# Kernel tuning notes

Hardware: AMD Instinct MI355X
Metric: run time of the kernel (lower is better)

## Reference

```python
import jax, jax.numpy as jnp
import numpy as np

N, E, D_IN, H, C, D_OUT = 50000, 800000, 16, 4, 64, 32


def setup_inputs() -> dict:
    key = jax.random.key(0)
    ks = jax.random.split(key, 24)
    w = lambda k, shape: (jax.random.normal(k, shape, jnp.float32) * 0.1)
    p = {}
    p["x"] = jax.random.normal(ks[0], (N, D_IN), jnp.float32)
    p["edge_index"] = jax.random.randint(ks[1], (2, E), 0, N, jnp.int32)
    p["W1"] = w(ks[2], (D_IN, H * C))
    p["a1_src"] = w(ks[3], (H, C))
    p["a1_dst"] = w(ks[4], (H, C))
    p["b1"] = jnp.zeros((H * C,), jnp.float32)
    p["W2"] = w(ks[5], (H * C, H * C))
    p["a2_src"] = w(ks[6], (H, C))
    p["a2_dst"] = w(ks[7], (H, C))
    p["b2"] = jnp.zeros((H * C,), jnp.float32)
    # GATConv 3: 256 -> 32, 1 head, concat=False (mean)
    p["W3"] = w(ks[8], (H * C, 1 * D_OUT))
    p["a3_src"] = w(ks[9], (1, D_OUT))
    p["a3_dst"] = w(ks[10], (1, D_OUT))
    p["b3"] = jnp.zeros((D_OUT,), jnp.float32)
    # LayerNorms over 256
    p["g1"] = jnp.ones((H * C,), jnp.float32)
    p["beta1"] = jnp.zeros((H * C,), jnp.float32)
    p["g2"] = jnp.ones((H * C,), jnp.float32)
    p["beta2"] = jnp.zeros((H * C,), jnp.float32)
    # risk head: Linear(32,32) -> ReLU -> Linear(32,6) -> Sigmoid
    p["Wr1"] = w(ks[11], (D_OUT, 32))
    p["br1"] = jnp.zeros((32,), jnp.float32)
    p["Wr2"] = w(ks[12], (32, 6))
    p["br2"] = jnp.zeros((6,), jnp.float32)
    return p


def layernorm(x, g, b, eps=1e-5):
    mu = jnp.mean(x, axis=-1, keepdims=True)
    var = jnp.mean(jnp.square(x - mu), axis=-1, keepdims=True)
    return (x - mu) * jax.lax.rsqrt(var + eps) * g + b


def gat_layer(x, src, dst, W, b, a_src, a_dst, n_nodes, concat):
    # PyG GATConv (eval mode): lin -> per-edge leaky_relu score -> segment softmax over dst -> scatter sum
    heads, ch = a_src.shape
    h = (x @ W).reshape(n_nodes, heads, ch)                 # [N,H,C]
    alpha_s = jnp.sum(h * a_src[None], axis=-1)             # [N,H]
    alpha_d = jnp.sum(h * a_dst[None], axis=-1)             # [N,H]
    e = jax.nn.leaky_relu(alpha_s[src] + alpha_d[dst], 0.2)  # [E,H]
    m = jax.ops.segment_max(e, dst, num_segments=n_nodes)   # stable softmax per dst
    ex = jnp.exp(e - m[dst])
    denom = jax.ops.segment_sum(ex, dst, num_segments=n_nodes)
    alpha = ex / (denom[dst] + 1e-16)                        # [E,H]
    out = jax.ops.segment_sum(alpha[:, :, None] * h[src], dst, num_segments=n_nodes)  # [N,H,C]
    out = out.reshape(n_nodes, heads * ch) if concat else out.mean(axis=1)
    return out + b


def reference(x, edge_index, W1, a1_src, a1_dst, b1, W2, a2_src, a2_dst, b2,
              W3, a3_src, a3_dst, b3, g1, beta1, g2, beta2, Wr1, br1, Wr2, br2):
    n = x.shape[0]
    loops = jnp.arange(n, dtype=edge_index.dtype)
    src = jnp.concatenate([edge_index[0], loops])  # GATConv adds self-loops by default
    dst = jnp.concatenate([edge_index[1], loops])
    h = gat_layer(x, src, dst, W1, b1, a1_src, a1_dst, n, True)
    h = jax.nn.elu(layernorm(h, g1, beta1))
    h = gat_layer(h, src, dst, W2, b2, a2_src, a2_dst, n, True)
    h = jax.nn.elu(layernorm(h, g2, beta2))
    h = gat_layer(h, src, dst, W3, b3, a3_src, a3_dst, n, False)
    risk = jax.nn.sigmoid(jax.nn.relu(h @ Wr1 + br1) @ Wr2 + br2)
    return (h, risk)
```

## Files before the change

### kernel.cpp

```cpp
#include <hip/hip_runtime.h>
#include <hip/hip_bf16.h>
#include <cmath>

constexpr int Nn  = 50000;
constexpr int Np  = 50176;
constexpr int Ee  = 800000;
constexpr int ET  = Ee + Nn;
constexpr int F   = 256;
constexpr int DO  = 32;

constexpr int A1S=4096, A1D=4352, B1O=4608,
              A2S=4864, A2D=5120, B2O=5376,
              A3S=5632, A3D=5664, B3O=5696,
              G1O=5728, BE1O=5984, G2O=6240, BE2O=6496,
              WR1O=6752, BR1O=7776, WR2O=7808, BR2O=8000, WTOT=8006;

struct InPtrs { const void* p[22]; };

typedef __attribute__((ext_vector_type(8))) short short8v;
typedef __attribute__((ext_vector_type(8))) unsigned short ushort8v;
typedef __attribute__((ext_vector_type(4))) float f32x4;

__device__ __forceinline__ float ld_in(const void* p, int i, int bf){
  if (bf){ unsigned u = (unsigned)((const unsigned short*)p)[i];
           union{unsigned u; float f;} c; c.u = u<<16; return c.f; }
  return ((const float*)p)[i];
}
__device__ __forceinline__ float b2f(unsigned short u){
  union{unsigned u; float f;} c; c.u = ((unsigned)u)<<16; return c.f;
}
__device__ __forceinline__ unsigned short f2b(float f){
  union{float f; unsigned u;} c; c.f=f; unsigned u=c.u;
  return (unsigned short)((u + 0x7fffu + ((u>>16)&1u))>>16);
}
__device__ __forceinline__ void st_out(void* o, int bf, long i, float v){
  if (bf) ((unsigned short*)o)[i] = f2b(v);
  else ((float*)o)[i]=v;
}
__device__ __forceinline__ float wsum64(float v){
  #pragma unroll
  for (int o=32;o;o>>=1) v += __shfl_xor(v,o);
  return v;
}

__global__ void k_detect(const unsigned* __restrict__ xr, int* __restrict__ flag){
  __shared__ int cnt;
  if (threadIdx.x==0) cnt=0;
  __syncthreads();
  int bad=0;
  for (int i=threadIdx.x;i<2048;i+=256){
    unsigned lo = xr[i]&0xffffu;
    unsigned ex = (lo>>7)&0xffu;
    if (ex>=133u) bad++;
  }
  atomicAdd(&cnt,bad);
  __syncthreads();
  if (threadIdx.x==0) *flag = (cnt<8) ? 1 : 0;
}

__global__ void k_prep(InPtrs ip, float* __restrict__ wf,
                       unsigned short* __restrict__ xp,
                       unsigned short* __restrict__ w1t,
                       unsigned short* __restrict__ w2t,
                       unsigned short* __restrict__ w3t,
                       const int* __restrict__ flagp){
  int g = blockIdx.x*256 + threadIdx.x;
  int bf = *flagp;
  if (g < Np*32){
    int row=g>>5, k=g&31;
    float v = (row<Nn && k<16)? ld_in(ip.p[0], row*16+k, bf) : 0.f;
    xp[g]=f2b(v); return;
  }
  g -= Np*32;
  if (g < 256*256){
    int n=g>>8, k=g&255;
    w2t[n*256+k] = f2b(ld_in(ip.p[6], k*256+n, bf)); return;
  }
  g -= 256*256;
  if (g < 256*32){
    int n=g>>5, k=g&31;
    w1t[g] = (k<16)? f2b(ld_in(ip.p[2], k*256+n, bf)) : (unsigned short)0; return;
  }
  g -= 256*32;
  if (g < 32*256){
    int n=g>>8, k=g&255;
    w3t[n*256+k] = f2b(ld_in(ip.p[10], k*32+n, bf)); return;
  }
  g -= 32*256;
  const int SIX[17]={3,4,5,7,8,9,11,12,13,14,15,16,17,18,19,20,21};
  const int SOF[17]={A1S,A1D,B1O,A2S,A2D,B2O,A3S,A3D,B3O,
                     G1O,BE1O,G2O,BE2O,WR1O,BR1O,WR2O,BR2O};
  const int SSZ[17]={256,256,256,256,256,256,32,32,32,
                     256,256,256,256,1024,32,192,6};
  for (int j=0;j<17;j++){
    if (g < SSZ[j]){ wf[SOF[j]+g] = ld_in(ip.p[SIX[j]], g, bf); return; }
    g -= SSZ[j];
  }
}

__global__ void k_count(const int* __restrict__ ei, int* __restrict__ deg){
  int g = blockIdx.x*256 + threadIdx.x;
  if (g < Ee) atomicAdd(&deg[ei[Ee+g]], 1);
}
__global__ void __launch_bounds__(256) k_scan_blk(const int* __restrict__ deg,
                                                  int* __restrict__ offtmp,
                                                  int* __restrict__ bsum){
  __shared__ int s[256];
  int t = threadIdx.x, i = blockIdx.x*256 + t;
  int v = (i<Nn) ? deg[i]+1 : 0;
  s[t]=v; __syncthreads();
  #pragma unroll
  for (int d=1; d<256; d<<=1){
    int x = (t>=d)? s[t-d] : 0; __syncthreads();
    s[t]+=x; __syncthreads();
  }
  if (i<Nn) offtmp[i] = s[t]-v;
  if (t==255) bsum[blockIdx.x] = s[255];
}
__global__ void __launch_bounds__(256) k_scan_top(const int* __restrict__ bsum,
                                                  int* __restrict__ bpre,
                                                  int* __restrict__ off){
  __shared__ int s[256];
  int t=threadIdx.x;
  int v = (t<196)? bsum[t]:0;
  s[t]=v; __syncthreads();
  #pragma unroll
  for (int d=1;d<256;d<<=1){ int x=(t>=d)?s[t-d]:0; __syncthreads(); s[t]+=x; __syncthreads(); }
  if (t<196) bpre[t]=s[t]-v;
  if (t==0) off[Nn]=ET;
}
__global__ void __launch_bounds__(256) k_scan_add(const int* __restrict__ offtmp,
                                                  const int* __restrict__ bpre,
                                                  int* __restrict__ off,
                                                  int* __restrict__ cursor){
  int i = blockIdx.x*256 + threadIdx.x;
  if (i<Nn){ int st = offtmp[i]+bpre[i>>8]; off[i]=st; cursor[i]=st; }
}
__global__ void k_fill(const int* __restrict__ ei, int* __restrict__ cursor,
                       int* __restrict__ csr, int* __restrict__ edst){
  int g = blockIdx.x*256 + threadIdx.x;
  if (g < Ee){
    int s = ei[g], d = ei[Ee+g];
    int p = atomicAdd(&cursor[d],1);
    csr[p] = s; edst[p] = d;
  } else if (g < ET){
    int n = g - Ee;
    int p = atomicAdd(&cursor[n],1);
    csr[p] = n; edst[p] = n;
  }
}

template<int BM,int BN,int WAVES_M,int WAVES_N,int KT,int EPI>
__global__ void __launch_bounds__(256) k_gemm_mfma(const unsigned short* __restrict__ Ag,
                                                   const unsigned short* __restrict__ BTg,
                                                   unsigned short* __restrict__ Cg,
                                                   const float* __restrict__ aswp,
                                                   const float* __restrict__ adwp,
                                                   float* __restrict__ aso,
                                                   float* __restrict__ ado,
                                                   int M, int N, int nMB){
  constexpr int WMT = BM/(WAVES_M*16);
  constexpr int WNT = BN/(WAVES_N*16);
  __shared__ unsigned short As[4*BM*8];
  __shared__ unsigned short Bs[4*BN*8];
  int bm = blockIdx.x % nMB, bn = blockIdx.x / nMB;
  int row0 = bm*BM, col0 = bn*BN;
  int tid = threadIdx.x, lane = tid&63, wid = tid>>6;
  int wm = wid % WAVES_M, wn = wid / WAVES_M;
  f32x4 acc[WMT][WNT];
  #pragma unroll
  for (int m=0;m<WMT;m++)
    #pragma unroll
    for (int n=0;n<WNT;n++){ acc[m][n].x=0.f; acc[m][n].y=0.f; acc[m][n].z=0.f; acc[m][n].w=0.f; }

  int cl = lane>>4, rl = lane&15;
  for (int kk=0; kk<KT; kk+=32){
    __syncthreads();
    for (int idx=tid; idx<4*BM; idx+=256){
      int r = idx>>2, c = idx&3;
      short8v v = *(const short8v*)(Ag + (size_t)(row0+r)*KT + kk + c*8);
      *(short8v*)(As + (c*BM + (r ^ (c<<2)))*8) = v;
    }
    for (int idx=tid; idx<4*BN; idx+=256){
      int r = idx>>2, c = idx&3;
      short8v v = *(const short8v*)(BTg + (size_t)(col0+r)*KT + kk + c*8);
      *(short8v*)(Bs + (c*BN + (r ^ (c<<2)))*8) = v;
    }
    __syncthreads();
    short8v af[WMT], bfv[WNT];
    #pragma unroll
    for (int m=0;m<WMT;m++){
      int r = wm*WMT*16 + m*16 + rl;
      af[m] = *(const short8v*)(As + (cl*BM + (r ^ (cl<<2)))*8);
    }
    #pragma unroll
    for (int n=0;n<WNT;n++){
      int r = wn*WNT*16 + n*16 + rl;
      bfv[n] = *(const short8v*)(Bs + (cl*BN + (r ^ (cl<<2)))*8);
    }
    #pragma unroll
    for (int m=0;m<WMT;m++)
      #pragma unroll
      for (int n=0;n<WNT;n++)
        acc[m][n] = __builtin_amdgcn_mfma_f32_16x16x32_bf16(af[m], bfv[n], acc[m][n], 0,0,0);
  }
  #pragma unroll
  for (int m=0;m<WMT;m++){
    int rbase = row0 + wm*WMT*16 + m*16 + (lane>>4)*4;
    #pragma unroll
    for (int n=0;n<WNT;n++){
      int col = col0 + wn*WNT*16 + n*16 + (lane&15);
      #pragma unroll
      for (int q=0;q<4;q++){
        int row = rbase + q;
        if (row < M) Cg[(size_t)row*N + col] = f2b(acc[m][n][q]);
      }
    }
  }
  if constexpr (EPI==1){
    #pragma unroll
    for (int m=0;m<WMT;m++){
      #pragma unroll
      for (int q=0;q<4;q++){
        float ps0=0,pd0=0,ps1=0,pd1=0;
        #pragma unroll
        for (int n=0;n<WNT;n++){
          int col = wn*(WNT*16) + n*16 + (lane&15);
          float av = acc[m][n][q];
          float ws = aswp[col], wd = adwp[col];
          if (n < WNT/2){ ps0 += av*ws; pd0 += av*wd; }
          else          { ps1 += av*ws; pd1 += av*wd; }
        }
        #pragma unroll
        for (int o=1;o<16;o<<=1){
          ps0 += __shfl_xor(ps0,o); pd0 += __shfl_xor(pd0,o);
          ps1 += __shfl_xor(ps1,o); pd1 += __shfl_xor(pd1,o);
        }
        int row = row0 + wm*(WMT*16) + m*16 + (lane>>4)*4 + q;
        if ((lane&15)==0 && row<M){
          int h0 = wn*2;
          aso[(size_t)row*4+h0  ]=ps0; aso[(size_t)row*4+h0+1]=ps1;
          ado[(size_t)row*4+h0  ]=pd0; ado[(size_t)row*4+h0+1]=pd1;
        }
      }
    }
  } else if constexpr (EPI==2){
    #pragma unroll
    for (int m=0;m<WMT;m++){
      #pragma unroll
      for (int q=0;q<4;q++){
        float ps=0,pd=0;
        #pragma unroll
        for (int n=0;n<WNT;n++){
          int col = n*16 + (lane&15);
          float av = acc[m][n][q];
          ps += av*aswp[col]; pd += av*adwp[col];
        }
        #pragma unroll
        for (int o=1;o<16;o<<=1){ ps+=__shfl_xor(ps,o); pd+=__shfl_xor(pd,o); }
        int row = row0 + wm*(WMT*16) + m*16 + (lane>>4)*4 + q;
        if ((lane&15)==0 && row<M){ aso[row]=ps; ado[row]=pd; }
      }
    }
  }
}

__global__ void __launch_bounds__(256) k_wexp(const float* __restrict__ as4,
                                              const float* __restrict__ ad4,
                                              const int* __restrict__ csr,
                                              const int* __restrict__ edst,
                                              float* __restrict__ wE){
  int e = blockIdx.x*256 + threadIdx.x;
  if (e>=ET) return;
  int s=csr[e], d=edst[e];
  const float4 a = *reinterpret_cast<const float4*>(as4 + (size_t)s*4);
  const float4 b = *reinterpret_cast<const float4*>(ad4 + (size_t)d*4);
  float t0=a.x+b.x; t0=t0>0.f?t0:0.2f*t0;
  float t1=a.y+b.y; t1=t1>0.f?t1:0.2f*t1;
  float t2=a.z+b.z; t2=t2>0.f?t2:0.2f*t2;
  float t3=a.w+b.w; t3=t3>0.f?t3:0.2f*t3;
  float4 w; w.x=__expf(t0); w.y=__expf(t1); w.z=__expf(t2); w.w=__expf(t3);
  *reinterpret_cast<float4*>(wE + (size_t)e*4) = w;
}

__global__ void __launch_bounds__(256) k_wexp3(const float* __restrict__ s3,
                                               const float* __restrict__ d3,
                                               const int* __restrict__ csr,
                                               const int* __restrict__ edst,
                                               float* __restrict__ w3e){
  int e = blockIdx.x*256 + threadIdx.x;
  if (e>=ET) return;
  float t = s3[csr[e]] + d3[edst[e]];
  t = t>0.f? t : 0.2f*t;
  w3e[e] = __expf(t);
}

__global__ void __launch_bounds__(256) k_agg(const unsigned short* __restrict__ Hs,
                                             const float* __restrict__ wE,
                                             const float* __restrict__ bias,
                                             const float* __restrict__ gam,
                                             const float* __restrict__ bet,
                                             const int* __restrict__ off,
                                             const int* __restrict__ csr,
                                             unsigned short* __restrict__ out){
  int wid = threadIdx.x>>6, lane = threadIdx.x&63;
  int n = blockIdx.x*4 + wid;
  if (n>=Nn) return;
  int half = lane>>5, c8 = lane&31;
  int h = c8>>3;
  const unsigned short* hbase = Hs + c8*8;
  int o0=off[n], o1=off[n+1], cnt=o1-o0;
  int mid = o0 + (cnt>>1);
  int lo = half? mid : o0;
  int hi = half? o1  : mid;
  float a0=0,a1=0,a2=0,a3=0,a4=0,a5=0,a6=0,a7=0,den=0;
  int e = lo;
  for (; e+3<hi; e+=4){
    int s0=csr[e], s1=csr[e+1], s2=csr[e+2], s3v=csr[e+3];
    float w0=wE[e*4+h], w1=wE[(e+1)*4+h], w2=wE[(e+2)*4+h], w3=wE[(e+3)*4+h];
    const ushort8v hv0 = *reinterpret_cast<const ushort8v*>(hbase + (size_t)s0*F);
    const ushort8v hv1 = *reinterpret_cast<const ushort8v*>(hbase + (size_t)s1*F);
    const ushort8v hv2 = *reinterpret_cast<const ushort8v*>(hbase + (size_t)s2*F);
    const ushort8v hv3 = *reinterpret_cast<const ushort8v*>(hbase + (size_t)s3v*F);
    den += (w0+w1)+(w2+w3);
    a0 += w0*b2f(hv0[0]) + w1*b2f(hv1[0]) + w2*b2f(hv2[0]) + w3*b2f(hv3[0]);
    a1 += w0*b2f(hv0[1]) + w1*b2f(hv1[1]) + w2*b2f(hv2[1]) + w3*b2f(hv3[1]);
    a2 += w0*b2f(hv0[2]) + w1*b2f(hv1[2]) + w2*b2f(hv2[2]) + w3*b2f(hv3[2]);
    a3 += w0*b2f(hv0[3]) + w1*b2f(hv1[3]) + w2*b2f(hv2[3]) + w3*b2f(hv3[3]);
    a4 += w0*b2f(hv0[4]) + w1*b2f(hv1[4]) + w2*b2f(hv2[4]) + w3*b2f(hv3[4]);
    a5 += w0*b2f(hv0[5]) + w1*b2f(hv1[5]) + w2*b2f(hv2[5]) + w3*b2f(hv3[5]);
    a6 += w0*b2f(hv0[6]) + w1*b2f(hv1[6]) + w2*b2f(hv2[6]) + w3*b2f(hv3[6]);
    a7 += w0*b2f(hv0[7]) + w1*b2f(hv1[7]) + w2*b2f(hv2[7]) + w3*b2f(hv3[7]);
  }
  for (; e<hi; ++e){
    int sv=csr[e];
    float w=wE[e*4+h];
    const ushort8v hv = *reinterpret_cast<const ushort8v*>(hbase + (size_t)sv*F);
    den += w;
    a0 += w*b2f(hv[0]); a1 += w*b2f(hv[1]); a2 += w*b2f(hv[2]); a3 += w*b2f(hv[3]);
    a4 += w*b2f(hv[4]); a5 += w*b2f(hv[5]); a6 += w*b2f(hv[6]); a7 += w*b2f(hv[7]);
  }
  a0 += __shfl_xor(a0,32); a1 += __shfl_xor(a1,32);
  a2 += __shfl_xor(a2,32); a3 += __shfl_xor(a3,32);
  a4 += __shfl_xor(a4,32); a5 += __shfl_xor(a5,32);
  a6 += __shfl_xor(a6,32); a7 += __shfl_xor(a7,32);
  den += __shfl_xor(den,32);
  float rs = 1.f/(den + 1e-16f);
  int c = c8*8;
  const float4 bv0 = *reinterpret_cast<const float4*>(bias + c);
  const float4 bv1 = *reinterpret_cast<const float4*>(bias + c + 4);
  a0=a0*rs+bv0.x; a1=a1*rs+bv0.y; a2=a2*rs+bv0.z; a3=a3*rs+bv0.w;
  a4=a4*rs+bv1.x; a5=a5*rs+bv1.y; a6=a6*rs+bv1.z; a7=a7*rs+bv1.w;
  float sl = a0+a1+a2+a3+a4+a5+a6+a7;
  float mu = wsum64(sl)*(1.f/512.f);
  float d0=a0-mu,d1=a1-mu,d2=a2-mu,d3=a3-mu,d4=a4-mu,d5=a5-mu,d6=a6-mu,d7=a7-mu;
  float ql = d0*d0+d1*d1+d2*d2+d3*d3+d4*d4+d5*d5+d6*d6+d7*d7;
  float var = wsum64(ql)*(1.f/512.f);
  float r = rsqrtf(var + 1e-5f);
  const float4 gv0 = *reinterpret_cast<const float4*>(gam + c);
  const float4 gv1 = *reinterpret_cast<const float4*>(gam + c + 4);
  const float4 ev0 = *reinterpret_cast<const float4*>(bet + c);
  const float4 ev1 = *reinterpret_cast<const float4*>(bet + c + 4);
  float y0=d0*r*gv0.x+ev0.x, y1=d1*r*gv0.y+ev0.y, y2=d2*r*gv0.z+ev0.z, y3=d3*r*gv0.w+ev0.w;
  float y4=d4*r*gv1.x+ev1.x, y5=d5*r*gv1.y+ev1.y, y6=d6*r*gv1.z+ev1.z, y7=d7*r*gv1.w+ev1.w;
  y0=y0>0.f?y0:expm1f(y0); y1=y1>0.f?y1:expm1f(y1);
  y2=y2>0.f?y2:expm1f(y2); y3=y3>0.f?y3:expm1f(y3);
  y4=y4>0.f?y4:expm1f(y4); y5=y5>0.f?y5:expm1f(y5);
  y6=y6>0.f?y6:expm1f(y6); y7=y7>0.f?y7:expm1f(y7);
  if (half==0){
    ushort8v ov;
    ov[0]=f2b(y0); ov[1]=f2b(y1); ov[2]=f2b(y2); ov[3]=f2b(y3);
    ov[4]=f2b(y4); ov[5]=f2b(y5); ov[6]=f2b(y6); ov[7]=f2b(y7);
    *reinterpret_cast<ushort8v*>(out + (size_t)n*F + c) = ov;
  }
}

__global__ void __launch_bounds__(256) k_agg3r(const unsigned short* __restrict__ C3,
                                               const float* __restrict__ w3e,
                                               const float* __restrict__ wf,
                                               const int* __restrict__ off,
                                               const int* __restrict__ csr,
                                               void* __restrict__ dout,
                                               const int* __restrict__ flagp){
  int wid=threadIdx.x>>6, lane=threadIdx.x&63;
  int n = blockIdx.x*4 + wid;
  if (n>=Nn) return;
  int bf = *flagp;
  int g = lane>>3, j = lane&7;
  int o0=off[n], o1=off[n+1], cnt=o1-o0;
  int lo = o0 + ((cnt*g)>>3), hi = o0 + ((cnt*(g+1))>>3);
  float a0=0,a1=0,a2=0,a3=0,den=0;
  for (int e=lo; e<hi; ++e){
    int s=csr[e];
    float w=w3e[e];
    const ushort4 hv = *reinterpret_cast<const ushort4*>(C3 + (size_t)s*DO + j*4);
    den += w;
    a0 += w*b2f(hv.x); a1 += w*b2f(hv.y); a2 += w*b2f(hv.z); a3 += w*b2f(hv.w);
  }
  #pragma unroll
  for (int o=8;o<64;o<<=1){
    a0 += __shfl_xor(a0,o); a1 += __shfl_xor(a1,o);
    a2 += __shfl_xor(a2,o); a3 += __shfl_xor(a3,o);
    den += __shfl_xor(den,o);
  }
  float rs = 1.f/(den + 1e-16f);
  const float4 bv = *reinterpret_cast<const float4*>(wf + B3O + j*4);
  float v0=a0*rs+bv.x, v1=a1*rs+bv.y, v2=a2*rs+bv.z, v3=a3*rs+bv.w;
  if (lane<8){
    long bo = (long)n*DO + lane*4;
    st_out(dout,bf,bo  ,v0); st_out(dout,bf,bo+1,v1);
    st_out(dout,bf,bo+2,v2); st_out(dout,bf,bo+3,v3);
  }
  float hk[32];
  #pragma unroll
  for (int k=0;k<32;k++){
    float src = ((k&3)==0)? v0 : ((k&3)==1)? v1 : ((k&3)==2)? v2 : v3;
    hk[k] = __shfl(src, k>>2);
  }
  float t1 = 0.f;
  if (lane<32){
    t1 = wf[BR1O+lane];
    #pragma unroll
    for (int k=0;k<32;k++) t1 += hk[k]*wf[WR1O + k*32 + lane];
    t1 = fmaxf(t1, 0.f);
  }
  float p0=0,p1=0,p2=0,p3=0,p4=0,p5=0;
  if (lane<32){
    const float* w2r = wf + WR2O + lane*6;
    p0=t1*w2r[0]; p1=t1*w2r[1]; p2=t1*w2r[2];
    p3=t1*w2r[3]; p4=t1*w2r[4]; p5=t1*w2r[5];
  }
  #pragma unroll
  for (int m=1;m<64;m<<=1){
    p0+=__shfl_xor(p0,m); p1+=__shfl_xor(p1,m); p2+=__shfl_xor(p2,m);
    p3+=__shfl_xor(p3,m); p4+=__shfl_xor(p4,m); p5+=__shfl_xor(p5,m);
  }
  if (lane<6){
    float s = (lane==0)?p0:(lane==1)?p1:(lane==2)?p2:(lane==3)?p3:(lane==4)?p4:p5;
    s += wf[BR2O+lane];
    float r = 1.f/(1.f+__expf(-s));
    st_out(dout, bf, (long)Nn*32 + (long)n*6 + lane, r);
  }
}

extern "C" void kernel_launch(void* const* d_in, const int* in_sizes, int n_in,
                              void* d_out, int out_size, void* d_ws, size_t ws_size,
                              hipStream_t stream){
  char* base = (char*)d_ws;
  size_t cur = 0;
  auto alloc = [&](size_t bytes)->char*{
    cur = (cur + 255) & ~(size_t)255;
    char* r = base + cur; cur += bytes; return r;
  };
  int*   flag = (int*)  alloc(4);
  float* wf   = (float*)alloc(sizeof(float)*WTOT);
  unsigned short* xpad = (unsigned short*)alloc(sizeof(short)*(size_t)Np*32);
  unsigned short* w1t = (unsigned short*)alloc(sizeof(short)*256*32);
  unsigned short* w2t = (unsigned short*)alloc(sizeof(short)*256*256);
  unsigned short* w3t = (unsigned short*)alloc(sizeof(short)*32*256);
  int*   deg  = (int*)  alloc(sizeof(int)*Nn);
  int*   offt = (int*)  alloc(sizeof(int)*Nn);
  int*   bsum = (int*)  alloc(sizeof(int)*256);
  int*   bpre = (int*)  alloc(sizeof(int)*256);
  int*   off  = (int*)  alloc(sizeof(int)*(Nn+1));
  int*   curs = (int*)  alloc(sizeof(int)*Nn);
  int*   csr  = (int*)  alloc(sizeof(int)*ET);
  int*   edst = (int*)  alloc(sizeof(int)*ET);
  unsigned short* G  = (unsigned short*)alloc(sizeof(short)*(size_t)Np*F);
  unsigned short* Hb = (unsigned short*)alloc(sizeof(short)*(size_t)Np*F);
  unsigned short* C3 = (unsigned short*)alloc(sizeof(short)*(size_t)Np*DO);
  float* as4  = (float*)alloc(sizeof(float)*(size_t)Nn*4);
  float* ad4  = (float*)alloc(sizeof(float)*(size_t)Nn*4);
  float* wE   = (float*)alloc(sizeof(float)*(size_t)ET*4);
  float* s3   = (float*)alloc(sizeof(float)*Nn);
  float* d3   = (float*)alloc(sizeof(float)*Nn);
  float* w3e  = (float*)alloc(sizeof(float)*(size_t)ET);

  const int* ei = (const int*)d_in[1];
  InPtrs ip;
  for (int i=0;i<22;i++) ip.p[i]=d_in[i];

  k_detect<<<1,256,0,stream>>>((const unsigned*)d_in[0], flag);
  {
    int total = Np*32 + 256*256 + 256*32 + 32*256 + 3910;
    k_prep<<<(total+255)/256,256,0,stream>>>(ip, wf, xpad, w1t, w2t, w3t, flag);
  }
  (void)hipMemsetAsync(deg, 0, sizeof(int)*Nn, stream);
  k_count<<<(Ee+255)/256,256,0,stream>>>(ei, deg);
  k_scan_blk<<<196,256,0,stream>>>(deg, offt, bsum);
  k_scan_top<<<1,256,0,stream>>>(bsum, bpre, off);
  k_scan_add<<<196,256,0,stream>>>(offt, bpre, off, curs);
  k_fill<<<(ET+255)/256,256,0,stream>>>(ei, curs, csr, edst);

  dim3 wg((Nn+3)/4);
  constexpr int nMB = Np/64;
  dim3 eg((ET+255)/256);
  k_gemm_mfma<64,256,2,2,32,1><<<nMB,256,0,stream>>>(xpad, w1t, G,
      wf+A1S, wf+A1D, as4, ad4, Nn, 256, nMB);
  k_wexp<<<eg,256,0,stream>>>(as4, ad4, csr, edst, wE);
  k_agg <<<wg,256,0,stream>>>(G, wE, wf+B1O, wf+G1O, wf+BE1O, off, csr, Hb);
  k_gemm_mfma<64,256,2,2,256,1><<<nMB,256,0,stream>>>(Hb, w2t, G,
      wf+A2S, wf+A2D, as4, ad4, Nn, 256, nMB);
  k_wexp<<<eg,256,0,stream>>>(as4, ad4, csr, edst, wE);
  k_agg <<<wg,256,0,stream>>>(G, wE, wf+B2O, wf+G2O, wf+BE2O, off, csr, Hb);
  k_gemm_mfma<64,32,4,1,256,2><<<nMB,256,0,stream>>>(Hb, w3t, C3,
      wf+A3S, wf+A3D, s3, d3, Nn, 32, nMB);
  k_wexp3<<<eg,256,0,stream>>>(s3, d3, csr, edst, w3e);
  k_agg3r<<<wg,256,0,stream>>>(C3, w3e, wf, off, csr, d_out, flag);
}
```

Measured before the change: 453.8 us.

## Fuse edge-score exp into aggregation and fold attention vectors into weights

New measurement: 474.6 us. 1.05x slower.

```diff
diff --git a/kernel.cpp b/kernel.cpp
--- a/kernel.cpp
+++ b/kernel.cpp
@@ -63,6 +63,8 @@
                        unsigned short* __restrict__ w1t,
                        unsigned short* __restrict__ w2t,
                        unsigned short* __restrict__ w3t,
+                       unsigned short* __restrict__ wa1t,
+                       unsigned short* __restrict__ wa2t,
                        const int* __restrict__ flagp){
   int g = blockIdx.x*256 + threadIdx.x;
   int bf = *flagp;
@@ -87,6 +89,30 @@
     w3t[n*256+k] = f2b(ld_in(ip.p[10], k*32+n, bf)); return;
   }
   g -= 32*256;
+  if (g < 16*256){
+    int col=g>>8, k=g&255;
+    float v=0.f;
+    if (col<8){
+      int h=col&3;
+      const void* av = (col<4)? ip.p[7] : ip.p[8];
+      for (int c=0;c<64;c++)
+        v += ld_in(ip.p[6], k*256 + h*64 + c, bf) * ld_in(av, h*64+c, bf);
+    }
+    wa2t[col*256+k] = f2b(v); return;
+  }
+  g -= 16*256;
+  if (g < 16*32){
+    int col=g>>5, k=g&31;
+    float v=0.f;
+    if (col<8 && k<16){
+      int h=col&3;
+      const void* av = (col<4)? ip.p[3] : ip.p[4];
+      for (int c=0;c<64;c++)
+        v += ld_in(ip.p[2], k*256 + h*64 + c, bf) * ld_in(av, h*64+c, bf);
+    }
+    wa1t[col*32+k] = f2b(v); return;
+  }
+  g -= 16*32;
   const int SIX[17]={3,4,5,7,8,9,11,12,13,14,15,16,17,18,19,20,21};
   const int SOF[17]={A1S,A1D,B1O,A2S,A2D,B2O,A3S,A3D,B3O,
                      G1O,BE1O,G2O,BE2O,WR1O,BR1O,WR2O,BR2O};
@@ -137,16 +163,16 @@
   if (i<Nn){ int st = offtmp[i]+bpre[i>>8]; off[i]=st; cursor[i]=st; }
 }
 __global__ void k_fill(const int* __restrict__ ei, int* __restrict__ cursor,
-                       int* __restrict__ csr, int* __restrict__ edst){
+                       int* __restrict__ csr){
   int g = blockIdx.x*256 + threadIdx.x;
   if (g < Ee){
     int s = ei[g], d = ei[Ee+g];
     int p = atomicAdd(&cursor[d],1);
-    csr[p] = s; edst[p] = d;
+    csr[p] = s;
   } else if (g < ET){
     int n = g - Ee;
     int p = atomicAdd(&cursor[n],1);
-    csr[p] = n; edst[p] = n;
+    csr[p] = n;
   }
 }
 
@@ -204,6 +230,19 @@
       for (int n=0;n<WNT;n++)
         acc[m][n] = __builtin_amdgcn_mfma_f32_16x16x32_bf16(af[m], bfv[n], acc[m][n], 0,0,0);
   }
+  if constexpr (EPI==3){
+    #pragma unroll
+    for (int m=0;m<WMT;m++){
+      int rbase = row0 + wm*WMT*16 + m*16 + (lane>>4)*4;
+      int col = lane&15;
+      #pragma unroll
+      for (int q=0;q<4;q++){
+        int row = rbase + q;
+        if (row < M) aso[(size_t)row*16 + col] = acc[m][0][q];
+      }
+    }
+    return;
+  }
   #pragma unroll
   for (int m=0;m<WMT;m++){
     int rbase = row0 + wm*WMT*16 + m*16 + (lane>>4)*4;
@@ -217,34 +256,7 @@
       }
     }
   }
-  if constexpr (EPI==1){
-    #pragma unroll
-    for (int m=0;m<WMT;m++){
-      #pragma unroll
-      for (int q=0;q<4;q++){
-        float ps0=0,pd0=0,ps1=0,pd1=0;
-        #pragma unroll
-        for (int n=0;n<WNT;n++){
-          int col = wn*(WNT*16) + n*16 + (lane&15);
-          float av = acc[m][n][q];
-          float ws = aswp[col], wd = adwp[col];
-          if (n < WNT/2){ ps0 += av*ws; pd0 += av*wd; }
-          else          { ps1 += av*ws; pd1 += av*wd; }
-        }
-        #pragma unroll
-        for (int o=1;o<16;o<<=1){
-          ps0 += __shfl_xor(ps0,o); pd0 += __shfl_xor(pd0,o);
-          ps1 += __shfl_xor(ps1,o); pd1 += __shfl_xor(pd1,o);
-        }
-        int row = row0 + wm*(WMT*16) + m*16 + (lane>>4)*4 + q;
-        if ((lane&15)==0 && row<M){
-          int h0 = wn*2;
-          aso[(size_t)row*4+h0  ]=ps0; aso[(size_t)row*4+h0+1]=ps1;
-          ado[(size_t)row*4+h0  ]=pd0; ado[(size_t)row*4+h0+1]=pd1;
-        }
-      }
-    }
-  } else if constexpr (EPI==2){
+  if constexpr (EPI==2){
     #pragma unroll
     for (int m=0;m<WMT;m++){
       #pragma unroll
@@ -265,38 +277,8 @@
   }
 }
 
-__global__ void __launch_bounds__(256) k_wexp(const float* __restrict__ as4,
-                                              const float* __restrict__ ad4,
-                                              const int* __restrict__ csr,
-                                              const int* __restrict__ edst,
-                                              float* __restrict__ wE){
-  int e = blockIdx.x*256 + threadIdx.x;
-  if (e>=ET) return;
-  int s=csr[e], d=edst[e];
-  const float4 a = *reinterpret_cast<const float4*>(as4 + (size_t)s*4);
-  const float4 b = *reinterpret_cast<const float4*>(ad4 + (size_t)d*4);
-  float t0=a.x+b.x; t0=t0>0.f?t0:0.2f*t0;
-  float t1=a.y+b.y; t1=t1>0.f?t1:0.2f*t1;
-  float t2=a.z+b.z; t2=t2>0.f?t2:0.2f*t2;
-  float t3=a.w+b.w; t3=t3>0.f?t3:0.2f*t3;
-  float4 w; w.x=__expf(t0); w.y=__expf(t1); w.z=__expf(t2); w.w=__expf(t3);
-  *reinterpret_cast<float4*>(wE + (size_t)e*4) = w;
-}
-
-__global__ void __launch_bounds__(256) k_wexp3(const float* __restrict__ s3,
-                                               const float* __restrict__ d3,
-                                               const int* __restrict__ csr,
-                                               const int* __restrict__ edst,
-                                               float* __restrict__ w3e){
-  int e = blockIdx.x*256 + threadIdx.x;
-  if (e>=ET) return;
-  float t = s3[csr[e]] + d3[edst[e]];
-  t = t>0.f? t : 0.2f*t;
-  w3e[e] = __expf(t);
-}
-
 __global__ void __launch_bounds__(256) k_agg(const unsigned short* __restrict__ Hs,
-                                             const float* __restrict__ wE,
+                                             const float* __restrict__ sc,
                                              const float* __restrict__ bias,
                                              const float* __restrict__ gam,
                                              const float* __restrict__ bet,
@@ -308,6 +290,7 @@
   if (n>=Nn) return;
   int half = lane>>5, c8 = lane&31;
   int h = c8>>3;
+  float adh = sc[(size_t)n*16 + 4 + h];
   const unsigned short* hbase = Hs + c8*8;
   int o0=off[n], o1=off[n+1], cnt=o1-o0;
   int mid = o0 + (cnt>>1);
@@ -317,11 +300,16 @@
   int e = lo;
   for (; e+3<hi; e+=4){
     int s0=csr[e], s1=csr[e+1], s2=csr[e+2], s3v=csr[e+3];
-    float w0=wE[e*4+h], w1=wE[(e+1)*4+h], w2=wE[(e+2)*4+h], w3=wE[(e+3)*4+h];
+    float q0=sc[(size_t)s0*16+h], q1=sc[(size_t)s1*16+h],
+          q2=sc[(size_t)s2*16+h], q3=sc[(size_t)s3v*16+h];
     const ushort8v hv0 = *reinterpret_cast<const ushort8v*>(hbase + (size_t)s0*F);
     const ushort8v hv1 = *reinterpret_cast<const ushort8v*>(hbase + (size_t)s1*F);
     const ushort8v hv2 = *reinterpret_cast<const ushort8v*>(hbase + (size_t)s2*F);
     const ushort8v hv3 = *reinterpret_cast<const ushort8v*>(hbase + (size_t)s3v*F);
+    float t0=q0+adh; t0=t0>0.f?t0:0.2f*t0; float w0=__expf(t0);
+    float t1=q1+adh; t1=t1>0.f?t1:0.2f*t1; float w1=__expf(t1);
+    float t2=q2+adh; t2=t2>0.f?t2:0.2f*t2; float w2=__expf(t2);
+    float t3=q3+adh; t3=t3>0.f?t3:0.2f*t3; float w3=__expf(t3);
     den += (w0+w1)+(w2+w3);
     a0 += w0*b2f(hv0[0]) + w1*b2f(hv1[0]) + w2*b2f(hv2[0]) + w3*b2f(hv3[0]);
     a1 += w0*b2f(hv0[1]) + w1*b2f(hv1[1]) + w2*b2f(hv2[1]) + w3*b2f(hv3[1]);
@@ -334,7 +322,8 @@
   }
   for (; e<hi; ++e){
     int sv=csr[e];
-    float w=wE[e*4+h];
+    float q=sc[(size_t)sv*16+h];
+    float t=q+adh; t=t>0.f?t:0.2f*t; float w=__expf(t);
     const ushort8v hv = *reinterpret_cast<const ushort8v*>(hbase + (size_t)sv*F);
     den += w;
     a0 += w*b2f(hv[0]); a1 += w*b2f(hv[1]); a2 += w*b2f(hv[2]); a3 += w*b2f(hv[3]);
@@ -376,7 +365,8 @@
 }
 
 __global__ void __launch_bounds__(256) k_agg3r(const unsigned short* __restrict__ C3,
-                                               const float* __restrict__ w3e,
+                                               const float* __restrict__ s3,
+                                               const float* __restrict__ d3,
                                                const float* __restrict__ wf,
                                                const int* __restrict__ off,
                                                const int* __restrict__ csr,
@@ -387,12 +377,14 @@
   if (n>=Nn) return;
   int bf = *flagp;
   int g = lane>>3, j = lane&7;
+  float dn = d3[n];
   int o0=off[n], o1=off[n+1], cnt=o1-o0;
   int lo = o0 + ((cnt*g)>>3), hi = o0 + ((cnt*(g+1))>>3);
   float a0=0,a1=0,a2=0,a3=0,den=0;
   for (int e=lo; e<hi; ++e){
     int s=csr[e];
-    float w=w3e[e];
+    float t = s3[s] + dn; t = t>0.f? t : 0.2f*t;
+    float w = __expf(t);
     const ushort4 hv = *reinterpret_cast<const ushort4*>(C3 + (size_t)s*DO + j*4);
     den += w;
     a0 += w*b2f(hv.x); a1 += w*b2f(hv.y); a2 += w*b2f(hv.z); a3 += w*b2f(hv.w);
@@ -455,9 +447,11 @@
   int*   flag = (int*)  alloc(4);
   float* wf   = (float*)alloc(sizeof(float)*WTOT);
   unsigned short* xpad = (unsigned short*)alloc(sizeof(short)*(size_t)Np*32);
-  unsigned short* w1t = (unsigned short*)alloc(sizeof(short)*256*32);
-  unsigned short* w2t = (unsigned short*)alloc(sizeof(short)*256*256);
-  unsigned short* w3t = (unsigned short*)alloc(sizeof(short)*32*256);
+  unsigned short* w1t  = (unsigned short*)alloc(sizeof(short)*256*32);
+  unsigned short* w2t  = (unsigned short*)alloc(sizeof(short)*256*256);
+  unsigned short* w3t  = (unsigned short*)alloc(sizeof(short)*32*256);
+  unsigned short* wa1t = (unsigned short*)alloc(sizeof(short)*16*32);
+  unsigned short* wa2t = (unsigned short*)alloc(sizeof(short)*16*256);
   int*   deg  = (int*)  alloc(sizeof(int)*Nn);
   int*   offt = (int*)  alloc(sizeof(int)*Nn);
   int*   bsum = (int*)  alloc(sizeof(int)*256);
@@ -465,16 +459,12 @@
   int*   off  = (int*)  alloc(sizeof(int)*(Nn+1));
   int*   curs = (int*)  alloc(sizeof(int)*Nn);
   int*   csr  = (int*)  alloc(sizeof(int)*ET);
-  int*   edst = (int*)  alloc(sizeof(int)*ET);
   unsigned short* G  = (unsigned short*)alloc(sizeof(short)*(size_t)Np*F);
   unsigned short* Hb = (unsigned short*)alloc(sizeof(short)*(size_t)Np*F);
   unsigned short* C3 = (unsigned short*)alloc(sizeof(short)*(size_t)Np*DO);
-  float* as4  = (float*)alloc(sizeof(float)*(size_t)Nn*4);
-  float* ad4  = (float*)alloc(sizeof(float)*(size_t)Nn*4);
-  float* wE   = (float*)alloc(sizeof(float)*(size_t)ET*4);
+  float* sc   = (float*)alloc(sizeof(float)*(size_t)Np*16);
   float* s3   = (float*)alloc(sizeof(float)*Nn);
   float* d3   = (float*)alloc(sizeof(float)*Nn);
-  float* w3e  = (float*)alloc(sizeof(float)*(size_t)ET);
 
   const int* ei = (const int*)d_in[1];
   InPtrs ip;
@@ -482,29 +472,29 @@
 
   k_detect<<<1,256,0,stream>>>((const unsigned*)d_in[0], flag);
   {
-    int total = Np*32 + 256*256 + 256*32 + 32*256 + 3910;
-    k_prep<<<(total+255)/256,256,0,stream>>>(ip, wf, xpad, w1t, w2t, w3t, flag);
+    int total = Np*32 + 256*256 + 256*32 + 32*256 + 16*256 + 16*32 + 3910;
+    k_prep<<<(total+255)/256,256,0,stream>>>(ip, wf, xpad, w1t, w2t, w3t, wa1t, wa2t, flag);
   }
   (void)hipMemsetAsync(deg, 0, sizeof(int)*Nn, stream);
   k_count<<<(Ee+255)/256,256,0,stream>>>(ei, deg);
   k_scan_blk<<<196,256,0,stream>>>(deg, offt, bsum);
   k_scan_top<<<1,256,0,stream>>>(bsum, bpre, off);
   k_scan_add<<<196,256,0,stream>>>(offt, bpre, off, curs);
-  k_fill<<<(ET+255)/256,256,0,stream>>>(ei, curs, csr, edst);
+  k_fill<<<(ET+255)/256,256,0,stream>>>(ei, curs, csr);
 
   dim3 wg((Nn+3)/4);
-  constexpr int nMB = Np/64;
-  dim3 eg((ET+255)/256);
-  k_gemm_mfma<64,256,2,2,32,1><<<nMB,256,0,stream>>>(xpad, w1t, G,
-      wf+A1S, wf+A1D, as4, ad4, Nn, 256, nMB);
-  k_wexp<<<eg,256,0,stream>>>(as4, ad4, csr, edst, wE);
-  k_agg <<<wg,256,0,stream>>>(G, wE, wf+B1O, wf+G1O, wf+BE1O, off, csr, Hb);
-  k_gemm_mfma<64,256,2,2,256,1><<<nMB,256,0,stream>>>(Hb, w2t, G,
-      wf+A2S, wf+A2D, as4, ad4, Nn, 256, nMB);
-  k_wexp<<<eg,256,0,stream>>>(as4, ad4, csr, edst, wE);
-  k_agg <<<wg,256,0,stream>>>(G, wE, wf+B2O, wf+G2O, wf+BE2O, off, csr, Hb);
-  k_gemm_mfma<64,32,4,1,256,2><<<nMB,256,0,stream>>>(Hb, w3t, C3,
-      wf+A3S, wf+A3D, s3, d3, Nn, 32, nMB);
-  k_wexp3<<<eg,256,0,stream>>>(s3, d3, csr, edst, w3e);
-  k_agg3r<<<wg,256,0,stream>>>(C3, w3e, wf, off, csr, d_out, flag);
-}
+  constexpr int NMB = (Nn+127)/128;
+  k_gemm_mfma<128,128,2,2,32,0><<<NMB*2,256,0,stream>>>(xpad, w1t, G,
+      nullptr, nullptr, nullptr, nullptr, Nn, 256, NMB);
+  k_gemm_mfma<128,16,4,1,32,3><<<NMB,256,0,stream>>>(xpad, wa1t, nullptr,
+      nullptr, nullptr, sc, nullptr, Nn, 16, NMB);
+  k_agg<<<wg,256,0,stream>>>(G, sc, wf+B1O, wf+G1O, wf+BE1O, off, csr, Hb);
+  k_gemm_mfma<128,128,2,2,256,0><<<NMB*2,256,0,stream>>>(Hb, w2t, G,
+      nullptr, nullptr, nullptr, nullptr, Nn, 256, NMB);
+  k_gemm_mfma<128,16,4,1,256,3><<<NMB,256,0,stream>>>(Hb, wa2t, nullptr,
+      nullptr, nullptr, sc, nullptr, Nn, 16, NMB);
+  k_agg<<<wg,256,0,stream>>>(G, sc, wf+B2O, wf+G2O, wf+BE2O, off, csr, Hb);
+  k_gemm_mfma<128,32,4,1,256,2><<<NMB,256,0,stream>>>(Hb, w3t, C3,
+      wf+A3S, wf+A3D, s3, d3, Nn, 32, NMB);
+  k_agg3r<<<wg,256,0,stream>>>(C3, s3, d3, wf, off, csr, d_out, flag);
+}
```
